# Kernel tuning notes

Hardware: AMD Instinct MI355X
Metric: run time of the kernel (lower is better)

The kernel has to match this reference:

```python
import jax, jax.numpy as jnp
import numpy as np

D_HIDDEN = 512
N_HEADS = 8
D_HEAD = D_HIDDEN // N_HEADS
LAYER_IDX = 0
FACTOR = 0.5 / float(np.sqrt(D_HEAD))


def setup_inputs() -> dict:
    key = jax.random.key(0)
    ks = jax.random.split(key, 16)
    B, N, d = 4, 2048, D_HIDDEN
    s = 1.0 / float(np.sqrt(d))
    inp = {
        "H": jax.random.normal(ks[0], (B, N, d), jnp.float32),
        "V": jax.random.normal(ks[1], (B, N, 3, d), jnp.float32),
        "D": jax.random.normal(ks[2], (B, N, N), jnp.float32),
        "rbf": jax.random.normal(ks[3], (1, B, 1, N, N), jnp.float32),
        "mask": jnp.ones((B, N), jnp.int32),
        # learned parameters (torch nn.Linear: y = x @ W.T + b)
        "Wq": jax.random.normal(ks[4], (4 * d, d), jnp.float32) * s,
        "bq": jax.random.normal(ks[5], (4 * d,), jnp.float32) * s,
        "Wk": jax.random.normal(ks[6], (4 * d, d), jnp.float32) * s,
        "bk": jax.random.normal(ks[7], (4 * d,), jnp.float32) * s,
        "Wv": jax.random.normal(ks[8], (d, d), jnp.float32) * s,
        "bv": jax.random.normal(ks[9], (d,), jnp.float32) * s,
        "Wvv": jax.random.normal(ks[10], (d, d), jnp.float32) * s,
        "Wo": jax.random.normal(ks[11], (d, d), jnp.float32) * s,
        "bo": jax.random.normal(ks[12], (d,), jnp.float32) * s,
        "Wvo": jax.random.normal(ks[13], (d, d), jnp.float32) * s,
    }
    return inp


def reference(H, V, D, rbf, mask, Wq, bq, Wk, bk, Wv, bv, Wvv, Wo, bo, Wvo):
    B, N, d = H.shape
    nh, dh = N_HEADS, D_HEAD
    # projections
    Hq = (H @ Wq.T + bq).reshape(B, N, nh, 4 * dh)
    Hk = (H @ Wk.T + bk).reshape(B, N, nh, 4 * dh)
    Hv = (H @ Wv.T + bv).reshape(B, N, nh, dh)
    # vector values: [B,N,3,nh,dh] -> [B,N,nh,3,dh] -> [B,N,nh,3*dh]
    Vv = (V @ Wvv.T).reshape(B, N, 3, nh, dh)
    Vv = jnp.swapaxes(Vv, -2, -3).reshape(B, N, nh, 3 * dh)
    V_attn = jnp.concatenate([Hv, Vv], axis=-1)  # [B,N,nh,4*dh]
    # additive geometric bias + key mask
    bias = rbf[LAYER_IDX] + D[:, None]  # [B,1,N,N]
    bias = jnp.where(mask[:, None, None, :] == 0, -jnp.inf, bias)
    # attention
    scores = jnp.einsum('bnhd,bmhd->bhnm', Hq, Hk) * FACTOR + bias
    attn = jax.nn.softmax(scores, axis=-1)
    res = jnp.einsum('bhnm,bmhd->bnhd', attn, V_attn)  # [B,N,nh,4*dh]
    # split scalar / vector outputs
    H_res = res[..., :dh].reshape(B, N, d)
    V_res = res[..., dh:].reshape(B, N, nh, 3, dh)
    V_res = jnp.swapaxes(V_res, -2, -3).reshape(B, N, 3, d)
    H_o = H_res @ Wo.T + bo
    V_o = V_res @ Wvo.T
    return H_o, V_o
```

## Files before the change

kernel.cpp:

```cpp
#include <hip/hip_runtime.h>
#include <hip/hip_bf16.h>
#include <stdint.h>

typedef __hip_bfloat16 bf16;
typedef __attribute__((ext_vector_type(8))) short bf16x8;
typedef __attribute__((ext_vector_type(4))) float f32x4;
typedef __attribute__((ext_vector_type(16))) float f32x16;
typedef __attribute__((ext_vector_type(4))) unsigned short u16x4;

#define DEVI __device__ __forceinline__

static constexpr float FACTOR = 0.0625f;

DEVI unsigned short bfbits(float x) {
  return __builtin_bit_cast(unsigned short, __float2bfloat16(x));
}
DEVI float b2f(unsigned short u) {
  return __builtin_bit_cast(float, (uint32_t)u << 16);
}

__global__ void cvt_plain(const float* __restrict__ src, bf16* __restrict__ dst, int n) {
  int i = (blockIdx.x * 256 + threadIdx.x) * 4;
  if (i >= n) return;
  float4 v = *reinterpret_cast<const float4*>(src + i);
  union { unsigned short u[4]; uint64_t d; } t;
  t.u[0] = bfbits(v.x); t.u[1] = bfbits(v.y); t.u[2] = bfbits(v.z); t.u[3] = bfbits(v.w);
  *reinterpret_cast<uint64_t*>(dst + i) = t.d;
}

__global__ void cvt_vperm(const float* __restrict__ src, bf16* __restrict__ dst) {
  int g = blockIdx.x * 256 + threadIdx.x;
  int k4  = (g & 127) * 4;
  int rem = g >> 7;
  int c  = rem % 3;
  int bn = rem / 3;
  float4 v = *reinterpret_cast<const float4*>(src + (size_t)rem * 512 + k4);
  union { unsigned short u[4]; uint64_t d; } t;
  t.u[0] = bfbits(v.x); t.u[1] = bfbits(v.y); t.u[2] = bfbits(v.z); t.u[3] = bfbits(v.w);
  *reinterpret_cast<uint64_t*>(dst + ((size_t)c * 8192 + bn) * 512 + k4) = t.d;
}

__global__ void cvt_weights(const float* __restrict__ wq, const float* __restrict__ wk,
                            const float* __restrict__ wv, const float* __restrict__ wvv,
                            const float* __restrict__ wo, const float* __restrict__ wvo,
                            bf16* __restrict__ dst) {
  int blk = blockIdx.x;
  const float* s; int off;
  if      (blk < 1024) { s = wq  + blk * 1024;          off = 0       + blk * 1024; }
  else if (blk < 2048) { s = wk  + (blk - 1024) * 1024; off = 1048576 + (blk - 1024) * 1024; }
  else if (blk < 2304) { s = wv  + (blk - 2048) * 1024; off = 2097152 + (blk - 2048) * 1024; }
  else if (blk < 2560) { s = wvv + (blk - 2304) * 1024; off = 2359296 + (blk - 2304) * 1024; }
  else if (blk < 2816) { s = wo  + (blk - 2560) * 1024; off = 2621440 + (blk - 2560) * 1024; }
  else                 { s = wvo + (blk - 2816) * 1024; off = 2883584 + (blk - 2816) * 1024; }
  int i = threadIdx.x * 4;
  float4 v = *reinterpret_cast<const float4*>(s + i);
  union { unsigned short u[4]; uint64_t d; } t;
  t.u[0] = bfbits(v.x); t.u[1] = bfbits(v.y); t.u[2] = bfbits(v.z); t.u[3] = bfbits(v.w);
  *reinterpret_cast<uint64_t*>(dst + off + i) = t.d;
}

__global__ void bias_combine(const float* __restrict__ D, const float* __restrict__ rbf,
                             const int* __restrict__ mask, bf16* __restrict__ Bc) {
  size_t i = ((size_t)blockIdx.x * 256 + threadIdx.x) * 4;
  int col = (int)(i & 2047);
  int b   = (int)(i >> 22);
  float4 d = *reinterpret_cast<const float4*>(D + i);
  float4 r = *reinterpret_cast<const float4*>(rbf + i);
  const int* mrow = mask + b * 2048 + col;
  union { unsigned short u[4]; uint64_t dd; } t;
  t.u[0] = mrow[0] ? bfbits(d.x + r.x) : bfbits(-1e30f);
  t.u[1] = mrow[1] ? bfbits(d.y + r.y) : bfbits(-1e30f);
  t.u[2] = mrow[2] ? bfbits(d.z + r.z) : bfbits(-1e30f);
  t.u[3] = mrow[3] ? bfbits(d.w + r.w) : bfbits(-1e30f);
  *reinterpret_cast<uint64_t*>(Bc + i) = t.dd;
}

template<int MODE>
__global__ __launch_bounds__(256, 2) void gemm_bt(const bf16* __restrict__ A,
                                                  const bf16* __restrict__ W,
                                                  const float* __restrict__ bias,
                                                  void* __restrict__ outp) {
  constexpr int K = 512;
  __shared__ bf16 As[128][40];
  __shared__ bf16 Bs[128][40];
  const int tid = threadIdx.x;
  const int wid = tid >> 6, lane = tid & 63;
  const int lr = lane & 15, lg = lane >> 4;
  const int wr = wid >> 1, wc = wid & 1;
  const int bm = blockIdx.y * 128, bn = blockIdx.x * 128;
  const int srow = tid >> 2;
  const int scol = (tid & 3) * 8;
  const bf16* Ap = A + (size_t)(bm + srow) * K + scol;
  const bf16* Wp = W + (size_t)(bn + srow) * K + scol;

  f32x4 acc[4][4];
#pragma unroll
  for (int m = 0; m < 4; m++)
#pragma unroll
    for (int n = 0; n < 4; n++) acc[m][n] = (f32x4){0.f, 0.f, 0.f, 0.f};

  bf16x8 a0 = *reinterpret_cast<const bf16x8*>(Ap);
  bf16x8 a1 = *reinterpret_cast<const bf16x8*>(Ap + 64 * K);
  bf16x8 b0 = *reinterpret_cast<const bf16x8*>(Wp);
  bf16x8 b1 = *reinterpret_cast<const bf16x8*>(Wp + 64 * K);

  for (int kt = 0; kt < 16; ++kt) {
    __syncthreads();
    *reinterpret_cast<bf16x8*>(&As[srow][scol])      = a0;
    *reinterpret_cast<bf16x8*>(&As[srow + 64][scol]) = a1;
    *reinterpret_cast<bf16x8*>(&Bs[srow][scol])      = b0;
    *reinterpret_cast<bf16x8*>(&Bs[srow + 64][scol]) = b1;
    __syncthreads();
    if (kt < 15) {
      a0 = *reinterpret_cast<const bf16x8*>(Ap + (kt + 1) * 32);
      a1 = *reinterpret_cast<const bf16x8*>(Ap + (kt + 1) * 32 + 64 * K);
      b0 = *reinterpret_cast<const bf16x8*>(Wp + (kt + 1) * 32);
      b1 = *reinterpret_cast<const bf16x8*>(Wp + (kt + 1) * 32 + 64 * K);
    }
    bf16x8 af[4], bfr[4];
#pragma unroll
    for (int m = 0; m < 4; m++)
      af[m] = *reinterpret_cast<const bf16x8*>(&As[wr * 64 + m * 16 + lr][lg * 8]);
#pragma unroll
    for (int n = 0; n < 4; n++)
      bfr[n] = *reinterpret_cast<const bf16x8*>(&Bs[wc * 64 + n * 16 + lr][lg * 8]);
#pragma unroll
    for (int m = 0; m < 4; m++)
#pragma unroll
      for (int n = 0; n < 4; n++)
        acc[m][n] = __builtin_amdgcn_mfma_f32_16x16x32_bf16(af[m], bfr[n], acc[m][n], 0, 0, 0);
  }

#pragma unroll
  for (int m = 0; m < 4; m++) {
#pragma unroll
    for (int n = 0; n < 4; n++) {
      const int col  = bn + wc * 64 + n * 16 + lr;
      const int row0 = bm + wr * 64 + m * 16 + lg * 4;
      if constexpr (MODE == 0 || MODE == 1) {
        bf16* out = (bf16*)outp;
        const float bb = bias[col];
        const int hh = col >> 8, t = col & 255;
#pragma unroll
        for (int q = 0; q < 4; q++) {
          const int row = row0 + q;
          const int b = row >> 11, nn = row & 2047;
          float v = acc[m][n][q] + bb;
          if constexpr (MODE == 0) v *= FACTOR;
          out[(size_t)((b * 8 + hh) * 2048 + nn) * 256 + t] = __float2bfloat16(v);
        }
      } else if constexpr (MODE == 2 || MODE == 3) {
        bf16* out = (bf16*)outp;
        const int hh = col >> 6, t = col & 63;
        int dimrow, b, nn;
        if constexpr (MODE == 2) {
          b = row0 >> 11; nn = row0 & 2047;
          dimrow = (b * 8 + hh) * 256 + t;
        } else {
          const int c = row0 >> 13; b = (row0 >> 11) & 3; nn = row0 & 2047;
          dimrow = (b * 8 + hh) * 256 + 64 + c * 64 + t;
        }
        const int i4 = (nn >> 2) & 7;
        const int o4 = (i4 & 4) | ((i4 & 1) << 1) | ((i4 >> 1) & 1);
        const int nn2 = (nn & ~31) | (o4 << 2);
        const float bb = (MODE == 2) ? bias[col] : 0.f;
        union { unsigned short u[4]; uint64_t d; } pk;
#pragma unroll
        for (int q = 0; q < 4; q++) pk.u[q] = bfbits(acc[m][n][q] + bb);
        *reinterpret_cast<uint64_t*>(out + (size_t)dimrow * 2048 + nn2) = pk.d;
      } else {
        float* out = (float*)outp;
        const float bb = (MODE == 4) ? bias[col] : 0.f;
#pragma unroll
        for (int q = 0; q < 4; q++) out[(size_t)(row0 + q) * 512 + col] = acc[m][n][q] + bb;
      }
    }
  }
}

__global__ __launch_bounds__(256, 2) void attn_kernel(
    const bf16* __restrict__ Qg, const bf16* __restrict__ Kg, const bf16* __restrict__ Vtg,
    const bf16* __restrict__ Bc, bf16* __restrict__ Hres, bf16* __restrict__ Vres) {
  __shared__ bf16 Ks[2][32 * 256];
  __shared__ bf16 Vs[2][256 * 32];

  const int g = blockIdx.x;
  const int x = g & 7, loc = g >> 3;
  const int bh = x * 4 + (loc & 3);
  const int qt = loc >> 2;
  const int b = bh >> 3, h = bh & 7;
  const int tid = threadIdx.x, w = tid >> 6, lane = tid & 63;
  const int lq = lane & 31, hi = lane >> 5;
  const int q0 = qt * 128 + w * 32;

  const bf16* Qb = Qg + (size_t)bh * 2048 * 256;
  const char* KbC = (const char*)(Kg + (size_t)bh * 2048 * 256);
  const char* VbC = (const char*)(Vtg + (size_t)bh * 256 * 2048);
  const bf16* Bb = Bc + ((size_t)(b * 2048 + q0 + lq)) * 2048 + hi * 4;

  bf16x8 qf[16];
#pragma unroll
  for (int kc = 0; kc < 16; kc++)
    qf[kc] = *reinterpret_cast<const bf16x8*>(Qb + (size_t)(q0 + lq) * 256 + kc * 16 + hi * 8);

  f32x16 O[8];
#pragma unroll
  for (int dt = 0; dt < 8; dt++)
#pragma unroll
    for (int r = 0; r < 16; r++) O[dt][r] = 0.f;
  float mrun = -INFINITY, lrun = 0.f;

  const char* ksrc[4]; const char* vsrc[4];
#pragma unroll
  for (int i = 0; i < 4; i++) {
    const int krow = w * 8 + 2 * i + hi;
    ksrc[i] = KbC + (size_t)krow * 512 + ((lq * 16) ^ ((krow & 31) << 4));
    const int vrow = w * 64 + i * 16 + (lane >> 2);
    const int gg = ((vrow >> 1) ^ (vrow >> 3)) & 3;
    vsrc[i] = VbC + (size_t)vrow * 4096 + (((lane & 3) ^ gg) << 4);
  }

  {
    char* dK = (char*)&Ks[0][0] + w * 4096;
    char* dV = (char*)&Vs[0][0] + w * 4096;
#pragma unroll
    for (int i = 0; i < 4; i++) {
      __builtin_amdgcn_global_load_lds(ksrc[i], dK + i * 1024, 16, 0, 0);
      __builtin_amdgcn_global_load_lds(vsrc[i], dV + i * 1024, 16, 0, 0);
    }
  }
  asm volatile("s_waitcnt vmcnt(0)" ::: "memory");
  __builtin_amdgcn_sched_barrier(0);
  __builtin_amdgcn_s_barrier();

  for (int kt = 0; kt < 64; ++kt) {
    const int cur = kt & 1;
    u16x4 bg[4];
#pragma unroll
    for (int i = 0; i < 4; i++)
      bg[i] = *reinterpret_cast<const u16x4*>(Bb + kt * 32 + i * 8);
    if (kt < 63) {
      char* dK = (char*)&Ks[cur ^ 1][0] + w * 4096;
      char* dV = (char*)&Vs[cur ^ 1][0] + w * 4096;
#pragma unroll
      for (int i = 0; i < 4; i++) {
        __builtin_amdgcn_global_load_lds(ksrc[i] + (size_t)(kt + 1) * 16384, dK + i * 1024, 16, 0, 0);
        __builtin_amdgcn_global_load_lds(vsrc[i] + (size_t)(kt + 1) * 64,    dV + i * 1024, 16, 0, 0);
      }
    }
    __builtin_amdgcn_sched_barrier(0);

    const char* KsC = (const char*)&Ks[cur][0];
    f32x16 s;
#pragma unroll
    for (int r = 0; r < 16; r++) s[r] = 0.f;
    const int kxor = lq << 4;
#pragma unroll
    for (int kc = 0; kc < 16; kc++) {
      bf16x8 kf = *reinterpret_cast<const bf16x8*>(KsC + lq * 512 + ((kc * 32 + hi * 16) ^ kxor));
      s = __builtin_amdgcn_mfma_f32_32x32x16_bf16(kf, qf[kc], s, 0, 0, 0);
    }
#pragma unroll
    for (int r = 0; r < 16; r++)
      s[r] += b2f((unsigned short)bg[r >> 2][r & 3]);

    float pmax = s[0];
#pragma unroll
    for (int r = 1; r < 16; r++) pmax = fmaxf(pmax, s[r]);
    pmax = fmaxf(pmax, __shfl_xor(pmax, 32));

    const float mnew = fmaxf(mrun, pmax);
    const float scq = __expf(mrun - mnew);
    mrun = mnew;
    lrun *= scq;
    float sfac[16];
#pragma unroll
    for (int r = 0; r < 16; r++) sfac[r] = __shfl(scq, (r & 3) + 8 * (r >> 2) + 4 * hi);
#pragma unroll
    for (int dt = 0; dt < 8; dt++)
#pragma unroll
      for (int r = 0; r < 16; r++) O[dt][r] *= sfac[r];

    union { unsigned short u[8]; bf16x8 v; } pa0, pa1;
    float rs = 0.f;
#pragma unroll
    for (int j = 0; j < 8; j++) {
      const float p = __expf(s[j] - mrun);
      pa0.u[j] = bfbits(p);
      rs += b2f(pa0.u[j]);
    }
#pragma unroll
    for (int j = 0; j < 8; j++) {
      const float p = __expf(s[8 + j] - mrun);
      pa1.u[j] = bfbits(p);
      rs += b2f(pa1.u[j]);
    }
    rs += __shfl_xor(rs, 32);
    lrun += rs;

    const char* VsC = (const char*)&Vs[cur][0];
#pragma unroll
    for (int dt = 0; dt < 8; dt++) {
      const int row = dt * 32 + lq;
      const int gg = ((row >> 1) ^ (row >> 3)) & 3;
      bf16x8 v0 = *reinterpret_cast<const bf16x8*>(VsC + row * 64 + ((hi ^ gg) << 4));
      bf16x8 v1 = *reinterpret_cast<const bf16x8*>(VsC + row * 64 + (((2 + hi) ^ gg) << 4));
      O[dt] = __builtin_amdgcn_mfma_f32_32x32x16_bf16(pa0.v, v0, O[dt], 0, 0, 0);
      O[dt] = __builtin_amdgcn_mfma_f32_32x32x16_bf16(pa1.v, v1, O[dt], 0, 0, 0);
    }

    if (kt < 63) {
      asm volatile("s_waitcnt vmcnt(0)" ::: "memory");
      __builtin_amdgcn_sched_barrier(0);
      __builtin_amdgcn_s_barrier();
    }
  }

  const float rli = 1.0f / lrun;
  float rl[16];
#pragma unroll
  for (int r = 0; r < 16; r++) rl[r] = __shfl(rli, (r & 3) + 8 * (r >> 2) + 4 * hi);
#pragma unroll
  for (int dt = 0; dt < 8; dt++) {
    const int d = dt * 32 + lq;
#pragma unroll
    for (int r = 0; r < 16; r++) {
      const int row = q0 + (r & 3) + 8 * (r >> 2) + 4 * hi;
      const float v = O[dt][r] * rl[r];
      if (d < 64) {
        Hres[(size_t)(b * 2048 + row) * 512 + h * 64 + d] = __float2bfloat16(v);
      } else {
        const int c = (d - 64) >> 6, t = (d - 64) & 63;
        Vres[((size_t)(b * 2048 + row) * 3 + c) * 512 + h * 64 + t] = __float2bfloat16(v);
      }
    }
  }
}

extern "C" void kernel_launch(void* const* d_in, const int* in_sizes, int n_in,
                              void* d_out, int out_size, void* d_ws, size_t ws_size,
                              hipStream_t stream) {
  const float* H   = (const float*)d_in[0];
  const float* V   = (const float*)d_in[1];
  const float* Dm  = (const float*)d_in[2];
  const float* rbf = (const float*)d_in[3];
  const int*   mask= (const int*)d_in[4];
  const float* Wq  = (const float*)d_in[5];
  const float* bq  = (const float*)d_in[6];
  const float* Wk  = (const float*)d_in[7];
  const float* bk  = (const float*)d_in[8];
  const float* Wv  = (const float*)d_in[9];
  const float* bv  = (const float*)d_in[10];
  const float* Wvv = (const float*)d_in[11];
  const float* Wo  = (const float*)d_in[12];
  const float* bo  = (const float*)d_in[13];
  const float* Wvo = (const float*)d_in[14];

  char* ws = (char*)d_ws;
  bf16* Hbf  = (bf16*)(ws);
  bf16* Vbf  = (bf16*)(ws + 8388608);
  bf16* Wall = (bf16*)(ws + 33554432);
  bf16* Qw   = (bf16*)(ws + 39845888);
  bf16* Kw   = (bf16*)(ws + 73400320);
  bf16* Vtw  = (bf16*)(ws + 106954752);
  bf16* Hres = Hbf;
  bf16* Vres = Vbf;
  bf16* Wqb  = Wall;
  bf16* Wkb  = Wall + 1048576;
  bf16* Wvb  = Wall + 2097152;
  bf16* Wvvb = Wall + 2359296;
  bf16* Wob  = Wall + 2621440;
  bf16* Wvob = Wall + 2883584;
  bf16* Bcb  = (bf16*)d_out;

  bias_combine<<<16384, 256, 0, stream>>>(Dm, rbf, mask, Bcb);
  cvt_plain<<<4096, 256, 0, stream>>>(H, Hbf, 4194304);
  cvt_vperm<<<12288, 256, 0, stream>>>(V, Vbf);
  cvt_weights<<<3072, 256, 0, stream>>>(Wq, Wk, Wv, Wvv, Wo, Wvo, Wall);

  gemm_bt<0><<<dim3(16, 64), 256, 0, stream>>>(Hbf, Wqb, bq, Qw);
  gemm_bt<1><<<dim3(16, 64), 256, 0, stream>>>(Hbf, Wkb, bk, Kw);
  gemm_bt<2><<<dim3(4, 64), 256, 0, stream>>>(Hbf, Wvb, bv, Vtw);
  gemm_bt<3><<<dim3(4, 192), 256, 0, stream>>>(Vbf, Wvvb, nullptr, Vtw);

  attn_kernel<<<512, 256, 0, stream>>>(Qw, Kw, Vtw, Bcb, Hres, Vres);

  gemm_bt<4><<<dim3(4, 64), 256, 0, stream>>>(Hres, Wob, bo, d_out);
  gemm_bt<5><<<dim3(4, 192), 256, 0, stream>>>(Vres, Wvob, nullptr, (float*)d_out + 4194304);
}
```

Baseline: 442.7 us.

## Merge projection GEMMs, async double-buffer GEMM loads, and optimize attention softmax loop

The six projection GEMM launches become three by concatenating the Q/K weights and stacking the H/V row blocks. Each GEMM now stages tiles through double-buffered LDS with direct global-to-LDS loads and an XOR swizzle, replacing register staging and two barriers per step. In attention, the bias tile is prefetched one iteration ahead and folded into the MFMA accumulator init. The softmax rescale is skipped lazily when the running max grows by at most 8, and setprio is raised around the MFMA blocks. Lazy rescaling lets unnormalized values grow by up to e^8, which is safe in fp32 but changes numerics slightly.

```diff
diff --git a/kernel.cpp b/kernel.cpp
--- a/kernel.cpp
+++ b/kernel.cpp
@@ -76,22 +76,32 @@
 }
 
 template<int MODE>
-__global__ __launch_bounds__(256, 2) void gemm_bt(const bf16* __restrict__ A,
-                                                  const bf16* __restrict__ W,
-                                                  const float* __restrict__ bias,
-                                                  void* __restrict__ outp) {
+__global__ __launch_bounds__(256, 2) void gemm2(const bf16* __restrict__ A,
+                                                const bf16* __restrict__ W,
+                                                const bf16* __restrict__ W2,
+                                                const float* __restrict__ bias,
+                                                const float* __restrict__ bias2,
+                                                void* __restrict__ outp) {
   constexpr int K = 512;
-  __shared__ bf16 As[128][40];
-  __shared__ bf16 Bs[128][40];
+  __shared__ bf16 As[2][4096];
+  __shared__ bf16 Bs[2][4096];
   const int tid = threadIdx.x;
   const int wid = tid >> 6, lane = tid & 63;
   const int lr = lane & 15, lg = lane >> 4;
   const int wr = wid >> 1, wc = wid & 1;
   const int bm = blockIdx.y * 128, bn = blockIdx.x * 128;
-  const int srow = tid >> 2;
-  const int scol = (tid & 3) * 8;
-  const bf16* Ap = A + (size_t)(bm + srow) * K + scol;
-  const bf16* Wp = W + (size_t)(bn + srow) * K + scol;
+
+  const bf16* Wp;
+  if constexpr (MODE == 0) Wp = W;
+  else Wp = (blockIdx.y < 64) ? W : W2;
+
+  const int q  = tid >> 2;
+  const int ch = ((tid & 3) ^ ((tid >> 3) & 3)) * 8;
+  const bf16* Asrc0 = A  + (size_t)(bm + q) * K + ch;
+  const bf16* Asrc1 = A  + (size_t)(bm + 64 + q) * K + ch;
+  const bf16* Wsrc0 = Wp + (size_t)(bn + q) * K + ch;
+  const bf16* Wsrc1 = Wp + (size_t)(bn + 64 + q) * K + ch;
+  const int wofs = wid * 1024;
 
   f32x4 acc[4][4];
 #pragma unroll
@@ -99,36 +109,41 @@
 #pragma unroll
     for (int n = 0; n < 4; n++) acc[m][n] = (f32x4){0.f, 0.f, 0.f, 0.f};
 
-  bf16x8 a0 = *reinterpret_cast<const bf16x8*>(Ap);
-  bf16x8 a1 = *reinterpret_cast<const bf16x8*>(Ap + 64 * K);
-  bf16x8 b0 = *reinterpret_cast<const bf16x8*>(Wp);
-  bf16x8 b1 = *reinterpret_cast<const bf16x8*>(Wp + 64 * K);
-
+  __builtin_amdgcn_global_load_lds((const char*)Asrc0, (char*)&As[0][0] + wofs,        16, 0, 0);
+  __builtin_amdgcn_global_load_lds((const char*)Asrc1, (char*)&As[0][0] + 4096 + wofs, 16, 0, 0);
+  __builtin_amdgcn_global_load_lds((const char*)Wsrc0, (char*)&Bs[0][0] + wofs,        16, 0, 0);
+  __builtin_amdgcn_global_load_lds((const char*)Wsrc1, (char*)&Bs[0][0] + 4096 + wofs, 16, 0, 0);
+  __syncthreads();
+
+  const int fxor = ((lr >> 1) & 3) << 4;
   for (int kt = 0; kt < 16; ++kt) {
-    __syncthreads();
-    *reinterpret_cast<bf16x8*>(&As[srow][scol])      = a0;
-    *reinterpret_cast<bf16x8*>(&As[srow + 64][scol]) = a1;
-    *reinterpret_cast<bf16x8*>(&Bs[srow][scol])      = b0;
-    *reinterpret_cast<bf16x8*>(&Bs[srow + 64][scol]) = b1;
-    __syncthreads();
+    const int cur = kt & 1;
     if (kt < 15) {
-      a0 = *reinterpret_cast<const bf16x8*>(Ap + (kt + 1) * 32);
-      a1 = *reinterpret_cast<const bf16x8*>(Ap + (kt + 1) * 32 + 64 * K);
-      b0 = *reinterpret_cast<const bf16x8*>(Wp + (kt + 1) * 32);
-      b1 = *reinterpret_cast<const bf16x8*>(Wp + (kt + 1) * 32 + 64 * K);
-    }
+      const int nxt = cur ^ 1;
+      __builtin_amdgcn_global_load_lds((const char*)(Asrc0 + (kt + 1) * 32), (char*)&As[nxt][0] + wofs,        16, 0, 0);
+      __builtin_amdgcn_global_load_lds((const char*)(Asrc1 + (kt + 1) * 32), (char*)&As[nxt][0] + 4096 + wofs, 16, 0, 0);
+      __builtin_amdgcn_global_load_lds((const char*)(Wsrc0 + (kt + 1) * 32), (char*)&Bs[nxt][0] + wofs,        16, 0, 0);
+      __builtin_amdgcn_global_load_lds((const char*)(Wsrc1 + (kt + 1) * 32), (char*)&Bs[nxt][0] + 4096 + wofs, 16, 0, 0);
+    }
+    const char* AsC = (const char*)&As[cur][0];
+    const char* BsC = (const char*)&Bs[cur][0];
     bf16x8 af[4], bfr[4];
 #pragma unroll
-    for (int m = 0; m < 4; m++)
-      af[m] = *reinterpret_cast<const bf16x8*>(&As[wr * 64 + m * 16 + lr][lg * 8]);
-#pragma unroll
-    for (int n = 0; n < 4; n++)
-      bfr[n] = *reinterpret_cast<const bf16x8*>(&Bs[wc * 64 + n * 16 + lr][lg * 8]);
+    for (int m = 0; m < 4; m++) {
+      const int row = wr * 64 + m * 16 + lr;
+      af[m] = *reinterpret_cast<const bf16x8*>(AsC + row * 64 + ((lg << 4) ^ fxor));
+    }
+#pragma unroll
+    for (int n = 0; n < 4; n++) {
+      const int row = wc * 64 + n * 16 + lr;
+      bfr[n] = *reinterpret_cast<const bf16x8*>(BsC + row * 64 + ((lg << 4) ^ fxor));
+    }
 #pragma unroll
     for (int m = 0; m < 4; m++)
 #pragma unroll
       for (int n = 0; n < 4; n++)
         acc[m][n] = __builtin_amdgcn_mfma_f32_16x16x32_bf16(af[m], bfr[n], acc[m][n], 0, 0, 0);
+    __syncthreads();
   }
 
 #pragma unroll
@@ -137,42 +152,53 @@
     for (int n = 0; n < 4; n++) {
       const int col  = bn + wc * 64 + n * 16 + lr;
       const int row0 = bm + wr * 64 + m * 16 + lg * 4;
-      if constexpr (MODE == 0 || MODE == 1) {
-        bf16* out = (bf16*)outp;
-        const float bb = bias[col];
-        const int hh = col >> 8, t = col & 255;
-#pragma unroll
-        for (int q = 0; q < 4; q++) {
-          const int row = row0 + q;
+      if constexpr (MODE == 0) {
+        const int isK = col >> 11;
+        const int col2 = col & 2047;
+        const float bb = isK ? bias2[col2] : bias[col2];
+        const int hh = col2 >> 8, t = col2 & 255;
+        bf16* out = (bf16*)outp + (size_t)isK * 16777216;
+#pragma unroll
+        for (int qq = 0; qq < 4; qq++) {
+          const int row = row0 + qq;
           const int b = row >> 11, nn = row & 2047;
-          float v = acc[m][n][q] + bb;
-          if constexpr (MODE == 0) v *= FACTOR;
+          float v = acc[m][n][qq] + bb;
+          if (!isK) v *= FACTOR;
           out[(size_t)((b * 8 + hh) * 2048 + nn) * 256 + t] = __float2bfloat16(v);
         }
-      } else if constexpr (MODE == 2 || MODE == 3) {
+      } else if constexpr (MODE == 1) {
         bf16* out = (bf16*)outp;
         const int hh = col >> 6, t = col & 63;
-        int dimrow, b, nn;
-        if constexpr (MODE == 2) {
-          b = row0 >> 11; nn = row0 & 2047;
+        int dimrow, nn; float bb;
+        if (row0 < 8192) {
+          const int b = row0 >> 11; nn = row0 & 2047;
           dimrow = (b * 8 + hh) * 256 + t;
+          bb = bias[col];
         } else {
-          const int c = row0 >> 13; b = (row0 >> 11) & 3; nn = row0 & 2047;
+          const int r = row0 - 8192;
+          const int c = r >> 13, b = (r >> 11) & 3; nn = r & 2047;
           dimrow = (b * 8 + hh) * 256 + 64 + c * 64 + t;
+          bb = 0.f;
         }
         const int i4 = (nn >> 2) & 7;
         const int o4 = (i4 & 4) | ((i4 & 1) << 1) | ((i4 >> 1) & 1);
         const int nn2 = (nn & ~31) | (o4 << 2);
-        const float bb = (MODE == 2) ? bias[col] : 0.f;
         union { unsigned short u[4]; uint64_t d; } pk;
 #pragma unroll
-        for (int q = 0; q < 4; q++) pk.u[q] = bfbits(acc[m][n][q] + bb);
+        for (int qq = 0; qq < 4; qq++) pk.u[qq] = bfbits(acc[m][n][qq] + bb);
         *reinterpret_cast<uint64_t*>(out + (size_t)dimrow * 2048 + nn2) = pk.d;
       } else {
         float* out = (float*)outp;
-        const float bb = (MODE == 4) ? bias[col] : 0.f;
-#pragma unroll
-        for (int q = 0; q < 4; q++) out[(size_t)(row0 + q) * 512 + col] = acc[m][n][q] + bb;
+        if (row0 < 8192) {
+          const float bb = bias[col];
+#pragma unroll
+          for (int qq = 0; qq < 4; qq++)
+            out[(size_t)(row0 + qq) * 512 + col] = acc[m][n][qq] + bb;
+        } else {
+#pragma unroll
+          for (int qq = 0; qq < 4; qq++)
+            out[4194304 + (size_t)(row0 - 8192 + qq) * 512 + col] = acc[m][n][qq];
+        }
       }
     }
   }
@@ -220,6 +246,9 @@
     vsrc[i] = VbC + (size_t)vrow * 4096 + (((lane & 3) ^ gg) << 4);
   }
 
+  u16x4 bg[4];
+#pragma unroll
+  for (int i = 0; i < 4; i++) bg[i] = *reinterpret_cast<const u16x4*>(Bb + i * 8);
   {
     char* dK = (char*)&Ks[0][0] + w * 4096;
     char* dV = (char*)&Vs[0][0] + w * 4096;
@@ -235,11 +264,13 @@
 
   for (int kt = 0; kt < 64; ++kt) {
     const int cur = kt & 1;
-    u16x4 bg[4];
-#pragma unroll
-    for (int i = 0; i < 4; i++)
-      bg[i] = *reinterpret_cast<const u16x4*>(Bb + kt * 32 + i * 8);
+    u16x4 bgn[4];
+#pragma unroll
+    for (int i = 0; i < 4; i++) bgn[i] = bg[i];
     if (kt < 63) {
+#pragma unroll
+      for (int i = 0; i < 4; i++)
+        bgn[i] = *reinterpret_cast<const u16x4*>(Bb + (kt + 1) * 32 + i * 8);
       char* dK = (char*)&Ks[cur ^ 1][0] + w * 4096;
       char* dV = (char*)&Vs[cur ^ 1][0] + w * 4096;
 #pragma unroll
@@ -253,33 +284,38 @@
     const char* KsC = (const char*)&Ks[cur][0];
     f32x16 s;
 #pragma unroll
-    for (int r = 0; r < 16; r++) s[r] = 0.f;
+    for (int r = 0; r < 16; r++) s[r] = b2f((unsigned short)bg[r >> 2][r & 3]);
     const int kxor = lq << 4;
+    __builtin_amdgcn_s_setprio(1);
 #pragma unroll
     for (int kc = 0; kc < 16; kc++) {
       bf16x8 kf = *reinterpret_cast<const bf16x8*>(KsC + lq * 512 + ((kc * 32 + hi * 16) ^ kxor));
       s = __builtin_amdgcn_mfma_f32_32x32x16_bf16(kf, qf[kc], s, 0, 0, 0);
     }
-#pragma unroll
-    for (int r = 0; r < 16; r++)
-      s[r] += b2f((unsigned short)bg[r >> 2][r & 3]);
-
-    float pmax = s[0];
-#pragma unroll
-    for (int r = 1; r < 16; r++) pmax = fmaxf(pmax, s[r]);
+    __builtin_amdgcn_s_setprio(0);
+
+    float m0 = fmaxf(s[0], s[1]),  m1 = fmaxf(s[2], s[3]);
+    float m2 = fmaxf(s[4], s[5]),  m3 = fmaxf(s[6], s[7]);
+    float m4 = fmaxf(s[8], s[9]),  m5 = fmaxf(s[10], s[11]);
+    float m6 = fmaxf(s[12], s[13]), m7 = fmaxf(s[14], s[15]);
+    float pmax = fmaxf(fmaxf(fmaxf(m0, m1), fmaxf(m2, m3)),
+                       fmaxf(fmaxf(m4, m5), fmaxf(m6, m7)));
     pmax = fmaxf(pmax, __shfl_xor(pmax, 32));
 
-    const float mnew = fmaxf(mrun, pmax);
-    const float scq = __expf(mrun - mnew);
-    mrun = mnew;
-    lrun *= scq;
-    float sfac[16];
-#pragma unroll
-    for (int r = 0; r < 16; r++) sfac[r] = __shfl(scq, (r & 3) + 8 * (r >> 2) + 4 * hi);
-#pragma unroll
-    for (int dt = 0; dt < 8; dt++)
-#pragma unroll
-      for (int r = 0; r < 16; r++) O[dt][r] *= sfac[r];
+    const bool ok = (pmax <= mrun + 8.f);
+    if (!__all((int)ok)) {
+      const float mnew = fmaxf(mrun, pmax);
+      const float scq = __expf(mrun - mnew);
+      mrun = mnew;
+      lrun *= scq;
+      float sfac[16];
+#pragma unroll
+      for (int r = 0; r < 16; r++) sfac[r] = __shfl(scq, (r & 3) + 8 * (r >> 2) + 4 * hi);
+#pragma unroll
+      for (int dt = 0; dt < 8; dt++)
+#pragma unroll
+        for (int r = 0; r < 16; r++) O[dt][r] *= sfac[r];
+    }
 
     union { unsigned short u[8]; bf16x8 v; } pa0, pa1;
     float rs = 0.f;
@@ -299,6 +335,7 @@
     lrun += rs;
 
     const char* VsC = (const char*)&Vs[cur][0];
+    __builtin_amdgcn_s_setprio(1);
 #pragma unroll
     for (int dt = 0; dt < 8; dt++) {
       const int row = dt * 32 + lq;
@@ -308,12 +345,15 @@
       O[dt] = __builtin_amdgcn_mfma_f32_32x32x16_bf16(pa0.v, v0, O[dt], 0, 0, 0);
       O[dt] = __builtin_amdgcn_mfma_f32_32x32x16_bf16(pa1.v, v1, O[dt], 0, 0, 0);
     }
+    __builtin_amdgcn_s_setprio(0);
 
     if (kt < 63) {
       asm volatile("s_waitcnt vmcnt(0)" ::: "memory");
       __builtin_amdgcn_sched_barrier(0);
       __builtin_amdgcn_s_barrier();
     }
+#pragma unroll
+    for (int i = 0; i < 4; i++) bg[i] = bgn[i];
   }
 
   const float rli = 1.0f / lrun;
@@ -358,15 +398,12 @@
 
   char* ws = (char*)d_ws;
   bf16* Hbf  = (bf16*)(ws);
-  bf16* Vbf  = (bf16*)(ws + 8388608);
   bf16* Wall = (bf16*)(ws + 33554432);
   bf16* Qw   = (bf16*)(ws + 39845888);
   bf16* Kw   = (bf16*)(ws + 73400320);
   bf16* Vtw  = (bf16*)(ws + 106954752);
   bf16* Hres = Hbf;
-  bf16* Vres = Vbf;
   bf16* Wqb  = Wall;
-  bf16* Wkb  = Wall + 1048576;
   bf16* Wvb  = Wall + 2097152;
   bf16* Wvvb = Wall + 2359296;
   bf16* Wob  = Wall + 2621440;
@@ -375,16 +412,13 @@
 
   bias_combine<<<16384, 256, 0, stream>>>(Dm, rbf, mask, Bcb);
   cvt_plain<<<4096, 256, 0, stream>>>(H, Hbf, 4194304);
-  cvt_vperm<<<12288, 256, 0, stream>>>(V, Vbf);
+  cvt_vperm<<<12288, 256, 0, stream>>>(V, Hbf + 4194304);
   cvt_weights<<<3072, 256, 0, stream>>>(Wq, Wk, Wv, Wvv, Wo, Wvo, Wall);
 
-  gemm_bt<0><<<dim3(16, 64), 256, 0, stream>>>(Hbf, Wqb, bq, Qw);
-  gemm_bt<1><<<dim3(16, 64), 256, 0, stream>>>(Hbf, Wkb, bk, Kw);
-  gemm_bt<2><<<dim3(4, 64), 256, 0, stream>>>(Hbf, Wvb, bv, Vtw);
-  gemm_bt<3><<<dim3(4, 192), 256, 0, stream>>>(Vbf, Wvvb, nullptr, Vtw);
-
-  attn_kernel<<<512, 256, 0, stream>>>(Qw, Kw, Vtw, Bcb, Hres, Vres);
-
-  gemm_bt<4><<<dim3(4, 64), 256, 0, stream>>>(Hres, Wob, bo, d_out);
-  gemm_bt<5><<<dim3(4, 192), 256, 0, stream>>>(Vres, Wvob, nullptr, (float*)d_out + 4194304);
-}
+  gemm2<0><<<dim3(32, 64), 256, 0, stream>>>(Hbf, Wqb, nullptr, bq, bk, Qw);
+  gemm2<1><<<dim3(4, 256), 256, 0, stream>>>(Hbf, Wvb, Wvvb, bv, nullptr, Vtw);
+
+  attn_kernel<<<512, 256, 0, stream>>>(Qw, Kw, Vtw, Bcb, Hres, Hbf + 4194304);
+
+  gemm2<2><<<dim3(4, 256), 256, 0, stream>>>(Hbf, Wob, Wvob, bo, nullptr, d_out);
+}
```

Result: slower. 469.6 us (+6.1%).
